# Kernel tuning notes

Measured on AMD Instinct MI355X. Metric: run time of the kernel, lower is better.

Reference implementation:

```python
import jax, jax.numpy as jnp
import numpy as np

N_NODES = 100000
N_EDGES = 1600000
N_GRAPHS = 2000
N_FEAT = 13


def gcn_conv(x, edge_index, W, b, n):
    """PyG GCNConv: h = D^{-1/2}(A+I)D^{-1/2} X W + b (add_self_loops, symmetric norm)."""
    h = x @ W  # [n, out]
    loop = jnp.arange(n, dtype=edge_index.dtype)
    src = jnp.concatenate([edge_index[0], loop])  # message sources (x_j)
    dst = jnp.concatenate([edge_index[1], loop])  # aggregation targets
    deg = jax.ops.segment_sum(jnp.ones_like(dst, dtype=h.dtype), dst, num_segments=n)
    dinv = jnp.where(deg > 0, jax.lax.rsqrt(jnp.maximum(deg, 1e-12)), 0.0)
    norm = dinv[src] * dinv[dst]  # [E+n]
    out = jax.ops.segment_sum(h[src] * norm[:, None], dst, num_segments=n)
    return out + b


def setup_inputs() -> dict:
    key = jax.random.key(0)
    ks = jax.random.split(key, 12)
    d = {}
    d["x"] = jax.random.normal(ks[0], (N_NODES, N_FEAT), dtype=jnp.float32)
    d["edge_index"] = jax.random.randint(ks[1], (2, N_EDGES), 0, N_NODES, dtype=jnp.int32)
    d["batch"] = jnp.sort(jax.random.randint(ks[2], (N_NODES,), 0, N_GRAPHS, dtype=jnp.int32))
    def lin(k, i, o):
        return jax.random.normal(k, (i, o), dtype=jnp.float32) * (1.0 / np.sqrt(i))
    d["W0"] = lin(ks[3], N_FEAT, 128); d["b0"] = jnp.zeros((128,), jnp.float32)
    d["W1"] = lin(ks[4], 128, 128);    d["b1"] = jnp.zeros((128,), jnp.float32)
    d["W2"] = lin(ks[5], 128, 128);    d["b2"] = jnp.zeros((128,), jnp.float32)
    d["Wf0"] = lin(ks[6], 128, 256);   d["bf0"] = jnp.zeros((256,), jnp.float32)
    d["Wf1"] = lin(ks[7], 256, 128);   d["bf1"] = jnp.zeros((128,), jnp.float32)
    d["Wo"] = lin(ks[8], 128, 1);      d["bo"] = jnp.zeros((1,), jnp.float32)
    return d


def reference(x, edge_index, batch, W0, b0, W1, b1, W2, b2, Wf0, bf0, Wf1, bf1, Wo, bo):
    n = x.shape[0]
    h = jax.nn.relu(gcn_conv(x, edge_index, W0, b0, n))
    h = jax.nn.relu(gcn_conv(h, edge_index, W1, b1, n))
    h = gcn_conv(h, edge_index, W2, b2, n)  # no relu after last conv
    # global mean pool over graphs
    cnt = jax.ops.segment_sum(jnp.ones((n,), h.dtype), batch, num_segments=N_GRAPHS)
    pooled = jax.ops.segment_sum(h, batch, num_segments=N_GRAPHS) / jnp.maximum(cnt, 1.0)[:, None]
    h = jax.nn.relu(pooled @ Wf0 + bf0)
    h = jax.nn.relu(h @ Wf1 + bf1)
    return h @ Wo + bo  # [N_GRAPHS, 1]
```

## Files before the change

kernel.cpp:

```cpp
#include <hip/hip_runtime.h>
#include <hip/hip_bf16.h>

#define N_NODES  100000
#define N_EDGES  1600000
#define N_GRAPHS 2000
#define N_FEAT   13
#define HID      128
#define NB       ((N_NODES + 127) / 128)
#define NBLK     128
#define N2       (NB * NBLK)

typedef __attribute__((ext_vector_type(8))) short bf16x8;
typedef __attribute__((ext_vector_type(4))) float f32x4;
typedef __attribute__((ext_vector_type(8))) unsigned short ushort8;

__global__ void k_hist1(const int* __restrict__ dst, int* __restrict__ counts, int E) {
    __shared__ int hist[NB];
    int k = blockIdx.x, t = threadIdx.x;
    for (int b = t; b < NB; b += 256) hist[b] = 0;
    __syncthreads();
    int epb = (E + NBLK - 1) / NBLK;
    int base = k * epb, lim = min(base + epb, E);
    for (int i = base + t; i < lim; i += 256) atomicAdd(&hist[dst[i] >> 7], 1);
    __syncthreads();
    for (int b = t; b < NB; b += 256) counts[k * NB + b] = hist[b];
}

__global__ void k_transp(const int* __restrict__ counts, int* __restrict__ countsT) {
    int i = blockIdx.x * 256 + threadIdx.x;
    if (i < N2) countsT[i] = counts[(i & (NBLK - 1)) * NB + (i >> 7)];
}

__global__ void k_scatter(const int* __restrict__ src, const int* __restrict__ dst,
                          const int* __restrict__ scT, unsigned int* __restrict__ bstore, int E) {
    __shared__ int cnt[NB];
    int k = blockIdx.x, t = threadIdx.x;
    for (int b = t; b < NB; b += 256) cnt[b] = 0;
    __syncthreads();
    int epb = (E + NBLK - 1) / NBLK;
    int base = k * epb, lim = min(base + epb, E);
    for (int i = base + t; i < lim; i += 256) {
        int d = dst[i];
        int b = d >> 7;
        int r = atomicAdd(&cnt[b], 1);
        bstore[scT[b * NBLK + k] + r] = ((unsigned int)src[i] << 7) | (unsigned int)(d & 127);
    }
}

__global__ void k_bhistx(const unsigned int* __restrict__ bstore, const int* __restrict__ scT,
                         const float* __restrict__ x, int* __restrict__ indeg,
                         float* __restrict__ dinv, float* __restrict__ xs, int n, int E) {
    __shared__ int cnt[128];
    int b = blockIdx.x, t = threadIdx.x;
    if (t < 128) cnt[t] = 0;
    __syncthreads();
    int start = scT[b * NBLK];
    int end = (b + 1 < NB) ? scT[(b + 1) * NBLK] : E;
    for (int i = start + t; i < end; i += 256) atomicAdd(&cnt[bstore[i] & 127], 1);
    __syncthreads();
    int node = b * 128 + t;
    if (t < 128 && node < n) {
        int c = cnt[t];
        indeg[node] = c;
        float dv = rsqrtf((float)(c + 1));
        dinv[node] = dv;
        float r[16];
#pragma unroll
        for (int k = 0; k < N_FEAT; k++) r[k] = dv * x[node * N_FEAT + k];
        r[13] = r[14] = r[15] = 0.f;
        float4* o = (float4*)&xs[(size_t)node * 16];
        o[0] = float4{r[0], r[1], r[2], r[3]};
        o[1] = float4{r[4], r[5], r[6], r[7]};
        o[2] = float4{r[8], r[9], r[10], r[11]};
        o[3] = float4{r[12], r[13], r[14], r[15]};
    }
}

__global__ void k_bfill(const unsigned int* __restrict__ bstore, const int* __restrict__ scT,
                        const int* __restrict__ off, int* __restrict__ csr, int n, int E) {
    __shared__ int cur[128];
    __shared__ int loff[128];
    int b = blockIdx.x, t = threadIdx.x;
    if (t < 128) {
        cur[t] = 0;
        int node = b * 128 + t;
        loff[t] = (node < n) ? off[node] : 0;
    }
    __syncthreads();
    int start = scT[b * NBLK];
    int end = (b + 1 < NB) ? scT[(b + 1) * NBLK] : E;
    for (int i = start + t; i < end; i += 256) {
        unsigned int e = bstore[i];
        int dl = e & 127;
        int p = loff[dl] + atomicAdd(&cur[dl], 1);
        csr[p] = (int)(e >> 7);
    }
}

__global__ void k_scan1(const int* __restrict__ in, int* __restrict__ out,
                        int* __restrict__ bsum, int n) {
    __shared__ int ts[256];
    int t = threadIdx.x;
    int base = blockIdx.x * 1024 + t * 4;
    int v0 = (base + 0 < n) ? in[base + 0] : 0;
    int v1 = (base + 1 < n) ? in[base + 1] : 0;
    int v2 = (base + 2 < n) ? in[base + 2] : 0;
    int v3 = (base + 3 < n) ? in[base + 3] : 0;
    int s = v0 + v1 + v2 + v3;
    ts[t] = s;
    __syncthreads();
    for (int o = 1; o < 256; o <<= 1) {
        int x = (t >= o) ? ts[t - o] : 0;
        __syncthreads();
        ts[t] += x;
        __syncthreads();
    }
    if (t == 255) bsum[blockIdx.x] = ts[255];
    int run = ts[t] - s;
    if (base + 0 < n) out[base + 0] = run; run += v0;
    if (base + 1 < n) out[base + 1] = run; run += v1;
    if (base + 2 < n) out[base + 2] = run; run += v2;
    if (base + 3 < n) out[base + 3] = run;
}

__global__ void k_scan_block(const int* __restrict__ in, int* __restrict__ out, int len) {
    __shared__ int ts[256];
    int t = threadIdx.x;
    int v[8];
    int s = 0;
#pragma unroll
    for (int j = 0; j < 8; j++) {
        int i = t * 8 + j;
        v[j] = (i < len) ? in[i] : 0;
        s += v[j];
    }
    ts[t] = s;
    __syncthreads();
    for (int o = 1; o < 256; o <<= 1) {
        int x = (t >= o) ? ts[t - o] : 0;
        __syncthreads();
        ts[t] += x;
        __syncthreads();
    }
    int run = ts[t] - s;
#pragma unroll
    for (int j = 0; j < 8; j++) {
        int i = t * 8 + j;
        if (i < len) out[i] = run;
        run += v[j];
    }
}

__global__ void k_scan3(int* __restrict__ out, const int* __restrict__ bpre, int n) {
    int i = blockIdx.x * 256 + threadIdx.x;
    if (i < n) out[i] += bpre[i >> 10];
}

__device__ __forceinline__ unsigned short f2bf(float f) {
    unsigned int b = __float_as_uint(f);
    b += 0x7fffu + ((b >> 16) & 1u);
    return (unsigned short)(b >> 16);
}

__device__ __forceinline__ void addrow8(float (&a)[8], uint4 v) {
    a[0] += __uint_as_float(v.x << 16);
    a[1] += __uint_as_float(v.x & 0xffff0000u);
    a[2] += __uint_as_float(v.y << 16);
    a[3] += __uint_as_float(v.y & 0xffff0000u);
    a[4] += __uint_as_float(v.z << 16);
    a[5] += __uint_as_float(v.z & 0xffff0000u);
    a[6] += __uint_as_float(v.w << 16);
    a[7] += __uint_as_float(v.w & 0xffff0000u);
}

__global__ __launch_bounds__(256) void k_gf13(const float* __restrict__ xs,
                                              const int* __restrict__ off,
                                              const int* __restrict__ indeg,
                                              const int* __restrict__ csr,
                                              const float* __restrict__ dinv,
                                              const float* __restrict__ W,
                                              const float* __restrict__ b,
                                              unsigned short* __restrict__ h, int n) {
    __shared__ float Ws[N_FEAT * HID];
    __shared__ __align__(16) float aggs[64][16];
    __shared__ float bs[HID];
    int t = threadIdx.x;
    for (int i = t; i < N_FEAT * HID; i += 256) Ws[i] = W[i];
    if (t < HID) bs[t] = b[t];
    int lane = t & 63;
    int slot = (t >> 6) * 16 + (lane >> 2);
    int l2 = lane & 3;
    int nb = blockIdx.x * 64;
    int d = nb + slot;
    const float4* X4 = (const float4*)xs;
    if (d < n) {
        int s0 = off[d], c = indeg[d];
        float4 acc = X4[(size_t)d * 4 + l2];
        int p = 0;
        for (; p + 7 < c; p += 8) {
            int s_[8];
#pragma unroll
            for (int j = 0; j < 8; j++) s_[j] = csr[s0 + p + j];
            float4 v[8];
#pragma unroll
            for (int j = 0; j < 8; j++) v[j] = X4[(size_t)s_[j] * 4 + l2];
#pragma unroll
            for (int j = 0; j < 8; j++) {
                acc.x += v[j].x; acc.y += v[j].y; acc.z += v[j].z; acc.w += v[j].w;
            }
        }
        for (; p < c; p++) {
            float4 v = X4[(size_t)csr[s0 + p] * 4 + l2];
            acc.x += v.x; acc.y += v.y; acc.z += v.z; acc.w += v.w;
        }
        float dv = dinv[d];
        float4 r = {dv * acc.x, dv * acc.y, dv * acc.z, dv * acc.w};
        *(float4*)&aggs[slot][l2 * 4] = r;
    }
    __syncthreads();
    int f = t & 127;
    int g0 = t >> 7;
    float wreg[N_FEAT];
#pragma unroll
    for (int k = 0; k < N_FEAT; k++) wreg[k] = Ws[k * HID + f];
#pragma unroll
    for (int j = 0; j < 32; j++) {
        int nl = g0 + j * 2;
        int dd = nb + nl;
        if (dd < n) {
            float acc = bs[f];
#pragma unroll
            for (int k = 0; k < N_FEAT; k++) acc += aggs[nl][k] * wreg[k];
            h[(size_t)dd * HID + f] = f2bf(fmaxf(acc, 0.f));
        }
    }
}

__global__ void k_wcast2(const float* __restrict__ W1, const float* __restrict__ W2,
                         unsigned short* __restrict__ Wt1, unsigned short* __restrict__ Wt2) {
    int i = blockIdx.x * 256 + threadIdx.x;
    if (i < HID * HID) {
        int c = i >> 7, k = i & 127;
        Wt1[i] = f2bf(W1[k * HID + c]);
        Wt2[i] = f2bf(W2[k * HID + c]);
    }
}

__global__ __launch_bounds__(256) void k_mfma128(const unsigned short* __restrict__ X,
                                                 const unsigned short* __restrict__ Wt,
                                                 const float* __restrict__ dinv,
                                                 unsigned short* __restrict__ ubf, int n) {
    int t = threadIdx.x;
    int wave = t >> 6, lane = t & 63;
    int lrow = lane & 15;
    int lk8 = (lane >> 4) * 8;
    int tile0 = blockIdx.x * 16 + wave * 4;

    f32x4 acc[4][8];
#pragma unroll
    for (int nt = 0; nt < 4; nt++)
#pragma unroll
        for (int ct = 0; ct < 8; ct++) acc[nt][ct] = f32x4{0.f, 0.f, 0.f, 0.f};

#pragma unroll
    for (int s = 0; s < 4; s++) {
        bf16x8 bfr[8];
#pragma unroll
        for (int ct = 0; ct < 8; ct++) {
            int col = ct * 16 + lrow;
            bfr[ct] = *(const bf16x8*)&Wt[col * HID + s * 32 + lk8];
        }
#pragma unroll
        for (int nt = 0; nt < 4; nt++) {
            int row = min((tile0 + nt) * 16 + lrow, n - 1);
            bf16x8 afr = *(const bf16x8*)&X[(size_t)row * HID + s * 32 + lk8];
#pragma unroll
            for (int ct = 0; ct < 8; ct++)
                acc[nt][ct] = __builtin_amdgcn_mfma_f32_16x16x32_bf16(afr, bfr[ct], acc[nt][ct], 0, 0, 0);
        }
    }

#pragma unroll
    for (int nt = 0; nt < 4; nt++) {
        int rbase = (tile0 + nt) * 16 + (lane >> 4) * 4;
#pragma unroll
        for (int r = 0; r < 4; r++) {
            int row = rbase + r;
            if (row < n) {
                float dv = dinv[row];
#pragma unroll
                for (int ct = 0; ct < 8; ct++)
                    ubf[(size_t)row * HID + ct * 16 + lrow] = f2bf(dv * acc[nt][ct][r]);
            }
        }
    }
}

__global__ void k_gather128(const unsigned int* __restrict__ ubf, const int* __restrict__ off,
                            const int* __restrict__ indeg, const int* __restrict__ csr,
                            const float* __restrict__ dinv, const float* __restrict__ bias,
                            unsigned short* __restrict__ yh, int n) {
    int t = threadIdx.x;
    int lane = t & 63;
    int quad = lane >> 4, l4 = lane & 15;
    int d = blockIdx.x * 16 + (t >> 6) * 4 + quad;
    if (d >= n) return;
    int s0 = off[d], c = indeg[d];
    const uint4* U = (const uint4*)ubf;

    uint4 sv = U[(size_t)d * 16 + l4];
    float a[8] = {0.f, 0.f, 0.f, 0.f, 0.f, 0.f, 0.f, 0.f};
    addrow8(a, sv);

    int p = 0;
    for (; p + 7 < c; p += 8) {
        int s_[8];
#pragma unroll
        for (int j = 0; j < 8; j++) s_[j] = csr[s0 + p + j];
        uint4 v[8];
#pragma unroll
        for (int j = 0; j < 8; j++) v[j] = U[(size_t)s_[j] * 16 + l4];
#pragma unroll
        for (int j = 0; j < 8; j++) addrow8(a, v[j]);
    }
    if (p + 3 < c) {
        int s_[4];
#pragma unroll
        for (int j = 0; j < 4; j++) s_[j] = csr[s0 + p + j];
        uint4 v[4];
#pragma unroll
        for (int j = 0; j < 4; j++) v[j] = U[(size_t)s_[j] * 16 + l4];
#pragma unroll
        for (int j = 0; j < 4; j++) addrow8(a, v[j]);
        p += 4;
    }
    for (; p < c; p++) addrow8(a, U[(size_t)csr[s0 + p] * 16 + l4]);

    float dv = dinv[d];
    float4 bb0 = *(const float4*)&bias[l4 * 8];
    float4 bb1 = *(const float4*)&bias[l4 * 8 + 4];
    float r[8];
    r[0] = dv * a[0] + bb0.x; r[1] = dv * a[1] + bb0.y;
    r[2] = dv * a[2] + bb0.z; r[3] = dv * a[3] + bb0.w;
    r[4] = dv * a[4] + bb1.x; r[5] = dv * a[5] + bb1.y;
    r[6] = dv * a[6] + bb1.z; r[7] = dv * a[7] + bb1.w;
    ushort8 hh;
#pragma unroll
    for (int j = 0; j < 8; j++) hh[j] = f2bf(fmaxf(r[j], 0.f));
    *(ushort8*)&yh[(size_t)d * HID + l4 * 8] = hh;
}

__global__ void k_gather128p(const unsigned int* __restrict__ ubf, const int* __restrict__ off,
                             const int* __restrict__ indeg, const int* __restrict__ csr,
                             const float* __restrict__ dinv, const float* __restrict__ bias,
                             const int* __restrict__ batch, float* __restrict__ pooledm, int n) {
    __shared__ __align__(16) float part[16][128];
    __shared__ int bid[16];
    int t = threadIdx.x;
    int lane = t & 63;
    int quad = lane >> 4, l4 = lane & 15;
    int slot = (t >> 6) * 4 + quad;
    int d = blockIdx.x * 16 + slot;
    const uint4* U = (const uint4*)ubf;
    if (d < n) {
        int s0 = off[d], c = indeg[d];
        uint4 sv = U[(size_t)d * 16 + l4];
        float a[8] = {0.f, 0.f, 0.f, 0.f, 0.f, 0.f, 0.f, 0.f};
        addrow8(a, sv);
        int p = 0;
        for (; p + 7 < c; p += 8) {
            int s_[8];
#pragma unroll
            for (int j = 0; j < 8; j++) s_[j] = csr[s0 + p + j];
            uint4 v[8];
#pragma unroll
            for (int j = 0; j < 8; j++) v[j] = U[(size_t)s_[j] * 16 + l4];
#pragma unroll
            for (int j = 0; j < 8; j++) addrow8(a, v[j]);
        }
        if (p + 3 < c) {
            int s_[4];
#pragma unroll
            for (int j = 0; j < 4; j++) s_[j] = csr[s0 + p + j];
            uint4 v[4];
#pragma unroll
            for (int j = 0; j < 4; j++) v[j] = U[(size_t)s_[j] * 16 + l4];
#pragma unroll
            for (int j = 0; j < 4; j++) addrow8(a, v[j]);
            p += 4;
        }
        for (; p < c; p++) addrow8(a, U[(size_t)csr[s0 + p] * 16 + l4]);

        float dv = dinv[d];
        float4 bb0 = *(const float4*)&bias[l4 * 8];
        float4 bb1 = *(const float4*)&bias[l4 * 8 + 4];
        float4 r0 = {dv * a[0] + bb0.x, dv * a[1] + bb0.y, dv * a[2] + bb0.z, dv * a[3] + bb0.w};
        float4 r1 = {dv * a[4] + bb1.x, dv * a[5] + bb1.y, dv * a[6] + bb1.z, dv * a[7] + bb1.w};
        *(float4*)&part[slot][l4 * 8] = r0;
        *(float4*)&part[slot][l4 * 8 + 4] = r1;
        if (l4 == 0) bid[slot] = batch[d];
    } else {
        if (l4 == 0) bid[slot] = -1;
    }
    __syncthreads();
    if (t < 128) {
        int f = t;
        float acc = 0.f;
        int g = -1;
        for (int j = 0; j < 16; j++) {
            int bj = bid[j];
            if (bj < 0) break;
            if (bj != g) {
                if (g >= 0) atomicAdd(&pooledm[g * HID + f], acc);
                g = bj; acc = 0.f;
            }
            acc += part[j][f];
        }
        if (g >= 0) atomicAdd(&pooledm[g * HID + f], acc);
    }
}

__global__ void k_cnt(const int* __restrict__ batch, int* __restrict__ cnt, int n) {
    int i = blockIdx.x * 256 + threadIdx.x;
    if (i < n) atomicAdd(&cnt[batch[i]], 1);
}

__global__ void k_fc0(const float* __restrict__ in, const int* __restrict__ cnt,
                      const float* __restrict__ W, const float* __restrict__ b,
                      float* __restrict__ out) {
    __shared__ float row[128];
    int g = blockIdx.x, t = threadIdx.x;
    if (t < 128) row[t] = in[g * 128 + t] * (1.f / (float)max(cnt[g], 1));
    __syncthreads();
    float acc = 0.f;
#pragma unroll 8
    for (int k = 0; k < 128; k++) acc += row[k] * W[k * 256 + t];
    acc += b[t];
    out[g * 256 + t] = fmaxf(acc, 0.f);
}

__global__ void k_fc1(const float* __restrict__ in, const float* __restrict__ W,
                      const float* __restrict__ b, float* __restrict__ out) {
    __shared__ float row[256];
    int g = blockIdx.x, t = threadIdx.x;
    row[t] = in[g * 256 + t];
    row[t + 128] = in[g * 256 + t + 128];
    __syncthreads();
    float acc = 0.f;
#pragma unroll 8
    for (int k = 0; k < 256; k++) acc += row[k] * W[k * 128 + t];
    acc += b[t];
    out[g * 128 + t] = fmaxf(acc, 0.f);
}

__global__ void k_fco(const float* __restrict__ in, const float* __restrict__ Wo,
                      const float* __restrict__ bo, float* __restrict__ out) {
    int g = blockIdx.x, t = threadIdx.x;
    float acc = in[g * 128 + t] * Wo[t] + in[g * 128 + 64 + t] * Wo[64 + t];
    for (int s = 32; s > 0; s >>= 1) acc += __shfl_down(acc, s);
    if (t == 0) out[g] = acc + bo[0];
}

extern "C" void kernel_launch(void* const* d_in, const int* in_sizes, int n_in,
                              void* d_out, int out_size, void* d_ws, size_t ws_size,
                              hipStream_t stream) {
    const float* x   = (const float*)d_in[0];
    const int* ei    = (const int*)d_in[1];
    const int* src   = ei;
    const int* dst   = ei + N_EDGES;
    const int* batch = (const int*)d_in[2];
    const float* W0 = (const float*)d_in[3];  const float* b0 = (const float*)d_in[4];
    const float* W1 = (const float*)d_in[5];  const float* b1 = (const float*)d_in[6];
    const float* W2 = (const float*)d_in[7];  const float* b2 = (const float*)d_in[8];
    const float* Wf0 = (const float*)d_in[9];  const float* bf0 = (const float*)d_in[10];
    const float* Wf1 = (const float*)d_in[11]; const float* bf1 = (const float*)d_in[12];
    const float* Wo = (const float*)d_in[13];  const float* bo = (const float*)d_in[14];
    float* out = (float*)d_out;

    char* w = (char*)d_ws;
    size_t o = 0;
    auto take = [&](size_t bytes) -> char* {
        char* p = w + o;
        o += (bytes + 255) & ~(size_t)255;
        return p;
    };
    int* indeg    = (int*)take((size_t)N_NODES * 4);
    int* off      = (int*)take((size_t)N_NODES * 4);
    int* counts   = (int*)take((size_t)N2 * 4);
    int* countsT  = (int*)take((size_t)N2 * 4);
    int* scT      = (int*)take((size_t)N2 * 4);
    int* bsum     = (int*)take(256 * 4);
    int* bpre     = (int*)take(256 * 4);
    int* csr      = (int*)take((size_t)N_EDGES * 4);
    float* dinv   = (float*)take((size_t)N_NODES * 4);
    int* cnt      = (int*)take((size_t)N_GRAPHS * 4);
    float* xs     = (float*)take((size_t)N_NODES * 16 * 4);
    unsigned short* hbf0 = (unsigned short*)take((size_t)N_NODES * HID * 2);
    unsigned short* hbf1 = (unsigned short*)take((size_t)N_NODES * HID * 2);
    unsigned short* ubf  = (unsigned short*)take((size_t)N_NODES * HID * 2);
    unsigned short* Wt1  = (unsigned short*)take((size_t)HID * HID * 2);
    unsigned short* Wt2  = (unsigned short*)take((size_t)HID * HID * 2);
    float* pooledm= (float*)take((size_t)N_GRAPHS * HID * 4);
    float* fc0    = (float*)take((size_t)N_GRAPHS * 256 * 4);
    float* fc1    = (float*)take((size_t)N_GRAPHS * HID * 4);
    unsigned int* bstore = (unsigned int*)ubf;

    hipMemsetAsync(cnt, 0, (size_t)N_GRAPHS * 4, stream);
    hipMemsetAsync(pooledm, 0, (size_t)N_GRAPHS * HID * 4, stream);

    k_hist1<<<NBLK, 256, 0, stream>>>(dst, counts, N_EDGES);
    k_transp<<<(N2 + 255) / 256, 256, 0, stream>>>(counts, countsT);
    int nb2 = (N2 + 1023) / 1024;
    k_scan1<<<nb2, 256, 0, stream>>>(countsT, scT, bsum, N2);
    k_scan_block<<<1, 256, 0, stream>>>(bsum, bpre, nb2);
    k_scan3<<<(N2 + 255) / 256, 256, 0, stream>>>(scT, bpre, N2);
    k_scatter<<<NBLK, 256, 0, stream>>>(src, dst, scT, bstore, N_EDGES);
    k_bhistx<<<NB, 256, 0, stream>>>(bstore, scT, x, indeg, dinv, xs, N_NODES, N_EDGES);
    int nb1 = (N_NODES + 1023) / 1024;
    k_scan1<<<nb1, 256, 0, stream>>>(indeg, off, bsum, N_NODES);
    k_scan_block<<<1, 256, 0, stream>>>(bsum, bpre, nb1);
    k_scan3<<<(N_NODES + 255) / 256, 256, 0, stream>>>(off, bpre, N_NODES);
    k_bfill<<<NB, 256, 0, stream>>>(bstore, scT, off, csr, N_NODES, N_EDGES);
    k_cnt<<<(N_NODES + 255) / 256, 256, 0, stream>>>(batch, cnt, N_NODES);
    k_wcast2<<<(HID * HID + 255) / 256, 256, 0, stream>>>(W1, W2, Wt1, Wt2);

    k_gf13<<<(N_NODES + 63) / 64, 256, 0, stream>>>(xs, off, indeg, csr, dinv, W0, b0, hbf0, N_NODES);
    k_mfma128<<<(N_NODES + 255) / 256, 256, 0, stream>>>(hbf0, Wt1, dinv, ubf, N_NODES);
    k_gather128<<<(N_NODES + 15) / 16, 256, 0, stream>>>((const unsigned int*)ubf, off, indeg, csr, dinv, b1, hbf1, N_NODES);
    k_mfma128<<<(N_NODES + 255) / 256, 256, 0, stream>>>(hbf1, Wt2, dinv, ubf, N_NODES);
    k_gather128p<<<(N_NODES + 15) / 16, 256, 0, stream>>>((const unsigned int*)ubf, off, indeg, csr, dinv, b2, batch, pooledm, N_NODES);

    k_fc0<<<N_GRAPHS, 256, 0, stream>>>(pooledm, cnt, Wf0, bf0, fc0);
    k_fc1<<<N_GRAPHS, 128, 0, stream>>>(fc0, Wf1, bf1, fc1);
    k_fco<<<N_GRAPHS, 64, 0, stream>>>(fc1, Wo, bo, out);
}
```

Measured before the change: 350.4 us.

## Fuse each GCN gather with the following 128x128 MFMA and merge the MLP head

The layer-0 aggregation and the layer-1 gather now write their activated bf16 rows into a swizzled LDS tile, and each block then runs the 128x128 MFMA transform on that tile directly. This removes the hbf0/hbf1 global round trips and two kernel launches. The three pooled-MLP kernels are merged into one per-graph kernel, which drops the fc0/fc1 buffers. In exchange, each MFMA tail now re-reads the weights per 64-node block, and the gather work is grouped four nodes per thread group, which may lower memory-level parallelism in the latency-bound gather.

```diff
diff --git a/kernel.cpp b/kernel.cpp
--- a/kernel.cpp
+++ b/kernel.cpp
@@ -173,17 +173,60 @@
     a[7] += __uint_as_float(v.w & 0xffff0000u);
 }
 
-__global__ __launch_bounds__(256) void k_gf13(const float* __restrict__ xs,
-                                              const int* __restrict__ off,
-                                              const int* __restrict__ indeg,
-                                              const int* __restrict__ csr,
-                                              const float* __restrict__ dinv,
-                                              const float* __restrict__ W,
-                                              const float* __restrict__ b,
-                                              unsigned short* __restrict__ h, int n) {
+__global__ void k_wcast2(const float* __restrict__ W1, const float* __restrict__ W2,
+                         unsigned short* __restrict__ Wt1, unsigned short* __restrict__ Wt2) {
+    int i = blockIdx.x * 256 + threadIdx.x;
+    if (i < HID * HID) {
+        int c = i >> 7, k = i & 127;
+        Wt1[i] = f2bf(W1[k * HID + c]);
+        Wt2[i] = f2bf(W2[k * HID + c]);
+    }
+}
+
+__device__ __forceinline__ void mfma_tail(const unsigned short* hl, const unsigned short* Wt,
+                                          const float* dinv, unsigned short* u, int nb, int n,
+                                          int t) {
+    int wave = t >> 6, lane = t & 63;
+    int lrow = lane & 15, kq = lane >> 4;
+    f32x4 acc[8];
+#pragma unroll
+    for (int ct = 0; ct < 8; ct++) acc[ct] = f32x4{0.f, 0.f, 0.f, 0.f};
+#pragma unroll
+    for (int s = 0; s < 4; s++) {
+        int row = wave * 16 + lrow;
+        int boff = (row * 256 + s * 64 + kq * 16) ^ ((lrow & 7) << 4);
+        bf16x8 afr = *(const bf16x8*)((const char*)hl + boff);
+#pragma unroll
+        for (int ct = 0; ct < 8; ct++) {
+            bf16x8 bfr = *(const bf16x8*)&Wt[(ct * 16 + lrow) * HID + s * 32 + kq * 8];
+            acc[ct] = __builtin_amdgcn_mfma_f32_16x16x32_bf16(afr, bfr, acc[ct], 0, 0, 0);
+        }
+    }
+#pragma unroll
+    for (int r = 0; r < 4; r++) {
+        int node = nb + wave * 16 + kq * 4 + r;
+        if (node < n) {
+            float dv = dinv[node];
+#pragma unroll
+            for (int ct = 0; ct < 8; ct++)
+                u[(size_t)node * HID + ct * 16 + lrow] = f2bf(dv * acc[ct][r]);
+        }
+    }
+}
+
+__global__ __launch_bounds__(256) void k_gf13m(const float* __restrict__ xs,
+                                               const int* __restrict__ off,
+                                               const int* __restrict__ indeg,
+                                               const int* __restrict__ csr,
+                                               const float* __restrict__ dinv,
+                                               const float* __restrict__ W,
+                                               const float* __restrict__ b,
+                                               const unsigned short* __restrict__ Wt1,
+                                               unsigned short* __restrict__ u1, int n) {
     __shared__ float Ws[N_FEAT * HID];
+    __shared__ float bs[HID];
     __shared__ __align__(16) float aggs[64][16];
-    __shared__ float bs[HID];
+    __shared__ __align__(16) unsigned short hl[64 * 128];
     int t = threadIdx.x;
     for (int i = t; i < N_FEAT * HID; i += 256) Ws[i] = W[i];
     if (t < HID) bs[t] = b[t];
@@ -218,136 +261,90 @@
         *(float4*)&aggs[slot][l2 * 4] = r;
     }
     __syncthreads();
-    int f = t & 127;
-    int g0 = t >> 7;
-    float wreg[N_FEAT];
-#pragma unroll
-    for (int k = 0; k < N_FEAT; k++) wreg[k] = Ws[k * HID + f];
-#pragma unroll
-    for (int j = 0; j < 32; j++) {
-        int nl = g0 + j * 2;
-        int dd = nb + nl;
-        if (dd < n) {
+    {
+        int f = t & 127;
+        int g0 = t >> 7;
+        float wreg[N_FEAT];
+#pragma unroll
+        for (int k = 0; k < N_FEAT; k++) wreg[k] = Ws[k * HID + f];
+#pragma unroll
+        for (int j = 0; j < 32; j++) {
+            int nl = g0 + j * 2;
             float acc = bs[f];
 #pragma unroll
             for (int k = 0; k < N_FEAT; k++) acc += aggs[nl][k] * wreg[k];
-            h[(size_t)dd * HID + f] = f2bf(fmaxf(acc, 0.f));
-        }
-    }
-}
-
-__global__ void k_wcast2(const float* __restrict__ W1, const float* __restrict__ W2,
-                         unsigned short* __restrict__ Wt1, unsigned short* __restrict__ Wt2) {
-    int i = blockIdx.x * 256 + threadIdx.x;
-    if (i < HID * HID) {
-        int c = i >> 7, k = i & 127;
-        Wt1[i] = f2bf(W1[k * HID + c]);
-        Wt2[i] = f2bf(W2[k * HID + c]);
-    }
-}
-
-__global__ __launch_bounds__(256) void k_mfma128(const unsigned short* __restrict__ X,
-                                                 const unsigned short* __restrict__ Wt,
-                                                 const float* __restrict__ dinv,
-                                                 unsigned short* __restrict__ ubf, int n) {
+            int boff = (nl * 256 + f * 2) ^ ((nl & 7) << 4);
+            *(unsigned short*)((char*)hl + boff) = f2bf(fmaxf(acc, 0.f));
+        }
+    }
+    __syncthreads();
+    mfma_tail(hl, Wt1, dinv, u1, nb, n, t);
+}
+
+__global__ __launch_bounds__(256) void k_gfm(const unsigned int* __restrict__ ubf,
+                                             const int* __restrict__ off,
+                                             const int* __restrict__ indeg,
+                                             const int* __restrict__ csr,
+                                             const float* __restrict__ dinv,
+                                             const float* __restrict__ bias,
+                                             const unsigned short* __restrict__ Wt2,
+                                             unsigned short* __restrict__ u2, int n) {
+    __shared__ __align__(16) unsigned short hl[64 * 128];
     int t = threadIdx.x;
-    int wave = t >> 6, lane = t & 63;
-    int lrow = lane & 15;
-    int lk8 = (lane >> 4) * 8;
-    int tile0 = blockIdx.x * 16 + wave * 4;
-
-    f32x4 acc[4][8];
-#pragma unroll
-    for (int nt = 0; nt < 4; nt++)
-#pragma unroll
-        for (int ct = 0; ct < 8; ct++) acc[nt][ct] = f32x4{0.f, 0.f, 0.f, 0.f};
-
-#pragma unroll
-    for (int s = 0; s < 4; s++) {
-        bf16x8 bfr[8];
-#pragma unroll
-        for (int ct = 0; ct < 8; ct++) {
-            int col = ct * 16 + lrow;
-            bfr[ct] = *(const bf16x8*)&Wt[col * HID + s * 32 + lk8];
-        }
-#pragma unroll
-        for (int nt = 0; nt < 4; nt++) {
-            int row = min((tile0 + nt) * 16 + lrow, n - 1);
-            bf16x8 afr = *(const bf16x8*)&X[(size_t)row * HID + s * 32 + lk8];
-#pragma unroll
-            for (int ct = 0; ct < 8; ct++)
-                acc[nt][ct] = __builtin_amdgcn_mfma_f32_16x16x32_bf16(afr, bfr[ct], acc[nt][ct], 0, 0, 0);
-        }
-    }
-
-#pragma unroll
-    for (int nt = 0; nt < 4; nt++) {
-        int rbase = (tile0 + nt) * 16 + (lane >> 4) * 4;
-#pragma unroll
-        for (int r = 0; r < 4; r++) {
-            int row = rbase + r;
-            if (row < n) {
-                float dv = dinv[row];
-#pragma unroll
-                for (int ct = 0; ct < 8; ct++)
-                    ubf[(size_t)row * HID + ct * 16 + lrow] = f2bf(dv * acc[nt][ct][r]);
-            }
-        }
-    }
-}
-
-__global__ void k_gather128(const unsigned int* __restrict__ ubf, const int* __restrict__ off,
-                            const int* __restrict__ indeg, const int* __restrict__ csr,
-                            const float* __restrict__ dinv, const float* __restrict__ bias,
-                            unsigned short* __restrict__ yh, int n) {
-    int t = threadIdx.x;
-    int lane = t & 63;
-    int quad = lane >> 4, l4 = lane & 15;
-    int d = blockIdx.x * 16 + (t >> 6) * 4 + quad;
-    if (d >= n) return;
-    int s0 = off[d], c = indeg[d];
+    int Q = t >> 4;
+    int l4 = t & 15;
+    int nb = blockIdx.x * 64;
     const uint4* U = (const uint4*)ubf;
-
-    uint4 sv = U[(size_t)d * 16 + l4];
-    float a[8] = {0.f, 0.f, 0.f, 0.f, 0.f, 0.f, 0.f, 0.f};
-    addrow8(a, sv);
-
-    int p = 0;
-    for (; p + 7 < c; p += 8) {
-        int s_[8];
-#pragma unroll
-        for (int j = 0; j < 8; j++) s_[j] = csr[s0 + p + j];
-        uint4 v[8];
-#pragma unroll
-        for (int j = 0; j < 8; j++) v[j] = U[(size_t)s_[j] * 16 + l4];
-#pragma unroll
-        for (int j = 0; j < 8; j++) addrow8(a, v[j]);
-    }
-    if (p + 3 < c) {
-        int s_[4];
-#pragma unroll
-        for (int j = 0; j < 4; j++) s_[j] = csr[s0 + p + j];
-        uint4 v[4];
-#pragma unroll
-        for (int j = 0; j < 4; j++) v[j] = U[(size_t)s_[j] * 16 + l4];
-#pragma unroll
-        for (int j = 0; j < 4; j++) addrow8(a, v[j]);
-        p += 4;
-    }
-    for (; p < c; p++) addrow8(a, U[(size_t)csr[s0 + p] * 16 + l4]);
-
-    float dv = dinv[d];
     float4 bb0 = *(const float4*)&bias[l4 * 8];
     float4 bb1 = *(const float4*)&bias[l4 * 8 + 4];
-    float r[8];
-    r[0] = dv * a[0] + bb0.x; r[1] = dv * a[1] + bb0.y;
-    r[2] = dv * a[2] + bb0.z; r[3] = dv * a[3] + bb0.w;
-    r[4] = dv * a[4] + bb1.x; r[5] = dv * a[5] + bb1.y;
-    r[6] = dv * a[6] + bb1.z; r[7] = dv * a[7] + bb1.w;
-    ushort8 hh;
-#pragma unroll
-    for (int j = 0; j < 8; j++) hh[j] = f2bf(fmaxf(r[j], 0.f));
-    *(ushort8*)&yh[(size_t)d * HID + l4 * 8] = hh;
+#pragma unroll
+    for (int i = 0; i < 4; i++) {
+        int slot = Q * 4 + i;
+        int d = nb + slot;
+        if (d < n) {
+            int s0 = off[d], c = indeg[d];
+            float a[8] = {0.f, 0.f, 0.f, 0.f, 0.f, 0.f, 0.f, 0.f};
+            addrow8(a, U[(size_t)d * 16 + l4]);
+            int p = 0;
+            for (; p + 7 < c; p += 8) {
+                int s_[8];
+#pragma unroll
+                for (int j = 0; j < 8; j++) s_[j] = csr[s0 + p + j];
+                uint4 v[8];
+#pragma unroll
+                for (int j = 0; j < 8; j++) v[j] = U[(size_t)s_[j] * 16 + l4];
+#pragma unroll
+                for (int j = 0; j < 8; j++) addrow8(a, v[j]);
+            }
+            if (p + 3 < c) {
+                int s_[4];
+#pragma unroll
+                for (int j = 0; j < 4; j++) s_[j] = csr[s0 + p + j];
+                uint4 v[4];
+#pragma unroll
+                for (int j = 0; j < 4; j++) v[j] = U[(size_t)s_[j] * 16 + l4];
+#pragma unroll
+                for (int j = 0; j < 4; j++) addrow8(a, v[j]);
+                p += 4;
+            }
+            for (; p < c; p++) addrow8(a, U[(size_t)csr[s0 + p] * 16 + l4]);
+
+            float dv = dinv[d];
+            ushort8 hh;
+            hh[0] = f2bf(fmaxf(dv * a[0] + bb0.x, 0.f));
+            hh[1] = f2bf(fmaxf(dv * a[1] + bb0.y, 0.f));
+            hh[2] = f2bf(fmaxf(dv * a[2] + bb0.z, 0.f));
+            hh[3] = f2bf(fmaxf(dv * a[3] + bb0.w, 0.f));
+            hh[4] = f2bf(fmaxf(dv * a[4] + bb1.x, 0.f));
+            hh[5] = f2bf(fmaxf(dv * a[5] + bb1.y, 0.f));
+            hh[6] = f2bf(fmaxf(dv * a[6] + bb1.z, 0.f));
+            hh[7] = f2bf(fmaxf(dv * a[7] + bb1.w, 0.f));
+            int boff = (slot * 256 + l4 * 16) ^ ((slot & 7) << 4);
+            *(ushort8*)((char*)hl + boff) = hh;
+        }
+    }
+    __syncthreads();
+    mfma_tail(hl, Wt2, dinv, u2, nb, n, t);
 }
 
 __global__ void k_gather128p(const unsigned int* __restrict__ ubf, const int* __restrict__ off,
@@ -364,9 +361,8 @@
     const uint4* U = (const uint4*)ubf;
     if (d < n) {
         int s0 = off[d], c = indeg[d];
-        uint4 sv = U[(size_t)d * 16 + l4];
         float a[8] = {0.f, 0.f, 0.f, 0.f, 0.f, 0.f, 0.f, 0.f};
-        addrow8(a, sv);
+        addrow8(a, U[(size_t)d * 16 + l4]);
         int p = 0;
         for (; p + 7 < c; p += 8) {
             int s_[8];
@@ -425,40 +421,36 @@
     if (i < n) atomicAdd(&cnt[batch[i]], 1);
 }
 
-__global__ void k_fc0(const float* __restrict__ in, const int* __restrict__ cnt,
-                      const float* __restrict__ W, const float* __restrict__ b,
-                      float* __restrict__ out) {
+__global__ void k_head(const float* __restrict__ pooledm, const int* __restrict__ cnt,
+                       const float* __restrict__ Wf0, const float* __restrict__ bf0,
+                       const float* __restrict__ Wf1, const float* __restrict__ bf1,
+                       const float* __restrict__ Wo, const float* __restrict__ bo,
+                       float* __restrict__ out) {
     __shared__ float row[128];
+    __shared__ float f0[256];
+    __shared__ float f1[128];
     int g = blockIdx.x, t = threadIdx.x;
-    if (t < 128) row[t] = in[g * 128 + t] * (1.f / (float)max(cnt[g], 1));
-    __syncthreads();
-    float acc = 0.f;
+    if (t < 128) row[t] = pooledm[g * 128 + t] * (1.f / (float)max(cnt[g], 1));
+    __syncthreads();
+    {
+        float acc = 0.f;
 #pragma unroll 8
-    for (int k = 0; k < 128; k++) acc += row[k] * W[k * 256 + t];
-    acc += b[t];
-    out[g * 256 + t] = fmaxf(acc, 0.f);
-}
-
-__global__ void k_fc1(const float* __restrict__ in, const float* __restrict__ W,
-                      const float* __restrict__ b, float* __restrict__ out) {
-    __shared__ float row[256];
-    int g = blockIdx.x, t = threadIdx.x;
-    row[t] = in[g * 256 + t];
-    row[t + 128] = in[g * 256 + t + 128];
-    __syncthreads();
-    float acc = 0.f;
+        for (int k = 0; k < 128; k++) acc += row[k] * Wf0[k * 256 + t];
+        f0[t] = fmaxf(acc + bf0[t], 0.f);
+    }
+    __syncthreads();
+    if (t < 128) {
+        float acc = 0.f;
 #pragma unroll 8
-    for (int k = 0; k < 256; k++) acc += row[k] * W[k * 128 + t];
-    acc += b[t];
-    out[g * 128 + t] = fmaxf(acc, 0.f);
-}
-
-__global__ void k_fco(const float* __restrict__ in, const float* __restrict__ Wo,
-                      const float* __restrict__ bo, float* __restrict__ out) {
-    int g = blockIdx.x, t = threadIdx.x;
-    float acc = in[g * 128 + t] * Wo[t] + in[g * 128 + 64 + t] * Wo[64 + t];
-    for (int s = 32; s > 0; s >>= 1) acc += __shfl_down(acc, s);
-    if (t == 0) out[g] = acc + bo[0];
+        for (int k = 0; k < 256; k++) acc += f0[k] * Wf1[k * 128 + t];
+        f1[t] = fmaxf(acc + bf1[t], 0.f);
+    }
+    __syncthreads();
+    if (t < 64) {
+        float acc = f1[t] * Wo[t] + f1[t + 64] * Wo[64 + t];
+        for (int s = 32; s > 0; s >>= 1) acc += __shfl_down(acc, s);
+        if (t == 0) out[g] = acc + bo[0];
+    }
 }
 
 extern "C" void kernel_launch(void* const* d_in, const int* in_sizes, int n_in,
@@ -495,15 +487,12 @@
     float* dinv   = (float*)take((size_t)N_NODES * 4);
     int* cnt      = (int*)take((size_t)N_GRAPHS * 4);
     float* xs     = (float*)take((size_t)N_NODES * 16 * 4);
-    unsigned short* hbf0 = (unsigned short*)take((size_t)N_NODES * HID * 2);
-    unsigned short* hbf1 = (unsigned short*)take((size_t)N_NODES * HID * 2);
-    unsigned short* ubf  = (unsigned short*)take((size_t)N_NODES * HID * 2);
+    unsigned short* ubfA = (unsigned short*)take((size_t)N_NODES * HID * 2);
+    unsigned short* ubfB = (unsigned short*)take((size_t)N_NODES * HID * 2);
     unsigned short* Wt1  = (unsigned short*)take((size_t)HID * HID * 2);
     unsigned short* Wt2  = (unsigned short*)take((size_t)HID * HID * 2);
     float* pooledm= (float*)take((size_t)N_GRAPHS * HID * 4);
-    float* fc0    = (float*)take((size_t)N_GRAPHS * 256 * 4);
-    float* fc1    = (float*)take((size_t)N_GRAPHS * HID * 4);
-    unsigned int* bstore = (unsigned int*)ubf;
+    unsigned int* bstore = (unsigned int*)ubfA;
 
     hipMemsetAsync(cnt, 0, (size_t)N_GRAPHS * 4, stream);
     hipMemsetAsync(pooledm, 0, (size_t)N_GRAPHS * HID * 4, stream);
@@ -524,13 +513,9 @@
     k_cnt<<<(N_NODES + 255) / 256, 256, 0, stream>>>(batch, cnt, N_NODES);
     k_wcast2<<<(HID * HID + 255) / 256, 256, 0, stream>>>(W1, W2, Wt1, Wt2);
 
-    k_gf13<<<(N_NODES + 63) / 64, 256, 0, stream>>>(xs, off, indeg, csr, dinv, W0, b0, hbf0, N_NODES);
-    k_mfma128<<<(N_NODES + 255) / 256, 256, 0, stream>>>(hbf0, Wt1, dinv, ubf, N_NODES);
-    k_gather128<<<(N_NODES + 15) / 16, 256, 0, stream>>>((const unsigned int*)ubf, off, indeg, csr, dinv, b1, hbf1, N_NODES);
-    k_mfma128<<<(N_NODES + 255) / 256, 256, 0, stream>>>(hbf1, Wt2, dinv, ubf, N_NODES);
-    k_gather128p<<<(N_NODES + 15) / 16, 256, 0, stream>>>((const unsigned int*)ubf, off, indeg, csr, dinv, b2, batch, pooledm, N_NODES);
-
-    k_fc0<<<N_GRAPHS, 256, 0, stream>>>(pooledm, cnt, Wf0, bf0, fc0);
-    k_fc1<<<N_GRAPHS, 128, 0, stream>>>(fc0, Wf1, bf1, fc1);
-    k_fco<<<N_GRAPHS, 64, 0, stream>>>(fc1, Wo, bo, out);
-}
+    k_gf13m<<<(N_NODES + 63) / 64, 256, 0, stream>>>(xs, off, indeg, csr, dinv, W0, b0, Wt1, ubfA, N_NODES);
+    k_gfm<<<(N_NODES + 63) / 64, 256, 0, stream>>>((const unsigned int*)ubfA, off, indeg, csr, dinv, b1, Wt2, ubfB, N_NODES);
+    k_gather128p<<<(N_NODES + 15) / 16, 256, 0, stream>>>((const unsigned int*)ubfB, off, indeg, csr, dinv, b2, batch, pooledm, N_NODES);
+
+    k_head<<<N_GRAPHS, 256, 0, stream>>>(pooledm, cnt, Wf0, bf0, Wf1, bf1, Wo, bo, out);
+}
```

Result: slower. 357.6 us (+2.0%).
